# Kernel tuning notes

Hardware: AMD Instinct MI355X
Metric: run time of the kernel (lower is better)

## Reference

```python
import jax, jax.numpy as jnp
import numpy as np

L, D, B, S = 131072, 512, 512, 512


def setup_inputs() -> dict:
    key = jax.random.key(0)
    k0, k1, k2, k3 = jax.random.split(key, 4)
    stdv = 1.0 / np.sqrt(D).astype(np.float32)
    inp = jax.random.normal(k0, (B, D), jnp.float32)
    labels = jax.random.normal(k1, (L, D), jnp.float32) * 0.05  # aggregated label embeddings 'v'
    weight = jax.random.uniform(k2, (L, D), jnp.float32, -stdv, stdv)  # refinement vectors 'u'
    alpha = jnp.zeros((1, D), jnp.float32)
    beta = jnp.zeros((1, D), jnp.float32)
    bias = jnp.zeros((L,), jnp.float32)
    shortlist = jax.random.randint(k3, (B, S), 0, L, dtype=jnp.int64)
    return {"input": inp, "labels": labels, "weight": weight,
            "alpha": alpha, "beta": beta, "bias": bias, "shortlist": shortlist}


def reference(input, labels, weight, alpha, beta, bias, shortlist):
    # sigmoid-gated combine of refinement vector u and label embedding v: [L, D]
    lbl_clf = jax.nn.sigmoid(alpha) * weight + jax.nn.sigmoid(beta) * labels
    # shortlist gather: [B, S, D] and [B, S]
    clf = lbl_clf[shortlist]
    b = bias[shortlist]
    # per-sample batched dot products: [B, S]
    out = jnp.einsum('bd,bsd->bs', input, clf) + b
    return out
```

## Files before the change

kernel.cpp:

```cpp
#include <hip/hip_runtime.h>


#define D_DIM 512
#define S_DIM 512

__global__ void combine_uv_kernel(
    const float* __restrict__ input,
    const float* __restrict__ labels,
    const float* __restrict__ weight,
    const float* __restrict__ alpha,
    const float* __restrict__ beta,
    const float* __restrict__ bias,
    const int* __restrict__ shortlist,
    float* __restrict__ out)
{
    __shared__ float ga[D_DIM];
    __shared__ float gb[D_DIM];
    __shared__ int sl[64];

    const int b   = blockIdx.x;
    const int s0  = blockIdx.y * 64;
    const int tid = threadIdx.x;

    for (int d = tid; d < D_DIM; d += 256) {
        float x  = input[b * D_DIM + d];
        float sa = 1.0f / (1.0f + __expf(-alpha[d]));
        float sb = 1.0f / (1.0f + __expf(-beta[d]));
        ga[d] = x * sa;
        gb[d] = x * sb;
    }
    if (tid < 64) sl[tid] = shortlist[b * S_DIM + s0 + tid];
    __syncthreads();

    const int wave = tid >> 6;
    const int lane = tid & 63;

    float a0[4], a1[4], b0v[4], b1v[4];
    #pragma unroll
    for (int k = 0; k < 4; ++k) {
        a0[k]  = ga[lane * 4 + k];
        a1[k]  = ga[256 + lane * 4 + k];
        b0v[k] = gb[lane * 4 + k];
        b1v[k] = gb[256 + lane * 4 + k];
    }

    for (int j = 0; j < 16; j += 2) {
        const int si0 = wave * 16 + j;
        const int si1 = si0 + 1;
        const long long l0 = (long long)sl[si0];
        const long long l1 = (long long)sl[si1];

        const float4* w0 = (const float4*)(weight + l0 * D_DIM);
        const float4* v0 = (const float4*)(labels + l0 * D_DIM);
        const float4* w1 = (const float4*)(weight + l1 * D_DIM);
        const float4* v1 = (const float4*)(labels + l1 * D_DIM);

        float4 w0a = w0[lane];      float4 w0b = w0[64 + lane];
        float4 v0a = v0[lane];      float4 v0b = v0[64 + lane];
        float4 w1a = w1[lane];      float4 w1b = w1[64 + lane];
        float4 v1a = v1[lane];      float4 v1b = v1[64 + lane];

        float acc0 = w0a.x * a0[0] + w0a.y * a0[1] + w0a.z * a0[2] + w0a.w * a0[3]
                   + w0b.x * a1[0] + w0b.y * a1[1] + w0b.z * a1[2] + w0b.w * a1[3]
                   + v0a.x * b0v[0] + v0a.y * b0v[1] + v0a.z * b0v[2] + v0a.w * b0v[3]
                   + v0b.x * b1v[0] + v0b.y * b1v[1] + v0b.z * b1v[2] + v0b.w * b1v[3];

        float acc1 = w1a.x * a0[0] + w1a.y * a0[1] + w1a.z * a0[2] + w1a.w * a0[3]
                   + w1b.x * a1[0] + w1b.y * a1[1] + w1b.z * a1[2] + w1b.w * a1[3]
                   + v1a.x * b0v[0] + v1a.y * b0v[1] + v1a.z * b0v[2] + v1a.w * b0v[3]
                   + v1b.x * b1v[0] + v1b.y * b1v[1] + v1b.z * b1v[2] + v1b.w * b1v[3];

        #pragma unroll
        for (int off = 32; off > 0; off >>= 1) {
            acc0 += __shfl_down(acc0, off, 64);
            acc1 += __shfl_down(acc1, off, 64);
        }

        if (lane == 0) {
            out[b * S_DIM + s0 + si0] = acc0 + bias[l0];
            out[b * S_DIM + s0 + si1] = acc1 + bias[l1];
        }
    }
}

extern "C" void kernel_launch(void* const* d_in, const int* in_sizes, int n_in,
                              void* d_out, int out_size, void* d_ws, size_t ws_size,
                              hipStream_t stream) {
    const float* input     = (const float*)d_in[0];
    const float* labels    = (const float*)d_in[1];
    const float* weight    = (const float*)d_in[2];
    const float* alpha     = (const float*)d_in[3];
    const float* beta      = (const float*)d_in[4];
    const float* bias      = (const float*)d_in[5];
    const int* shortlist   = (const int*)d_in[6];
    float* out             = (float*)d_out;

    const int B = 512;
    const int S = 512;
    dim3 grid(B, S / 64);
    dim3 block(256);
    combine_uv_kernel<<<grid, block, 0, stream>>>(
        input, labels, weight, alpha, beta, bias, shortlist, out);
}
```

Baseline: 571.6 us.

## Split each wave into 16-lane groups handling four shortlist rows concurrently

```diff
diff --git a/kernel.cpp b/kernel.cpp
--- a/kernel.cpp
+++ b/kernel.cpp
@@ -4,7 +4,8 @@
 #define D_DIM 512
 #define S_DIM 512
 
-__global__ void combine_uv_kernel(
+__global__ __launch_bounds__(256, 4)
+void combine_uv_kernel(
     const float* __restrict__ input,
     const float* __restrict__ labels,
     const float* __restrict__ weight,
@@ -16,7 +17,8 @@
 {
     __shared__ float ga[D_DIM];
     __shared__ float gb[D_DIM];
-    __shared__ int sl[64];
+    __shared__ int   sl[64];
+    __shared__ float bb[64];
 
     const int b   = blockIdx.x;
     const int s0  = blockIdx.y * 64;
@@ -29,57 +31,52 @@
         ga[d] = x * sa;
         gb[d] = x * sb;
     }
-    if (tid < 64) sl[tid] = shortlist[b * S_DIM + s0 + tid];
+    if (tid < 64) {
+        const int l = shortlist[b * S_DIM + s0 + tid];
+        sl[tid] = l;
+        bb[tid] = bias[l];
+    }
     __syncthreads();
 
     const int wave = tid >> 6;
     const int lane = tid & 63;
+    const int g    = lane >> 4;
+    const int m    = lane & 15;
 
-    float a0[4], a1[4], b0v[4], b1v[4];
+    const float4* gaf = (const float4*)ga;
+    const float4* gbf = (const float4*)gb;
+
     #pragma unroll
-    for (int k = 0; k < 4; ++k) {
-        a0[k]  = ga[lane * 4 + k];
-        a1[k]  = ga[256 + lane * 4 + k];
-        b0v[k] = gb[lane * 4 + k];
-        b1v[k] = gb[256 + lane * 4 + k];
-    }
+    for (int i = 0; i < 4; ++i) {
+        const int    si = wave * 16 + i * 4 + g;
+        const size_t l  = (size_t)sl[si];
+        const float4* wrow = (const float4*)(weight + l * D_DIM);
+        const float4* vrow = (const float4*)(labels + l * D_DIM);
 
-    for (int j = 0; j < 16; j += 2) {
-        const int si0 = wave * 16 + j;
-        const int si1 = si0 + 1;
-        const long long l0 = (long long)sl[si0];
-        const long long l1 = (long long)sl[si1];
+        float4 wd[8], vd[8];
+        #pragma unroll
+        for (int k = 0; k < 8; ++k) wd[k] = wrow[m + 16 * k];
+        #pragma unroll
+        for (int k = 0; k < 8; ++k) vd[k] = vrow[m + 16 * k];
 
-        const float4* w0 = (const float4*)(weight + l0 * D_DIM);
-        const float4* v0 = (const float4*)(labels + l0 * D_DIM);
-        const float4* w1 = (const float4*)(weight + l1 * D_DIM);
-        const float4* v1 = (const float4*)(labels + l1 * D_DIM);
-
-        float4 w0a = w0[lane];      float4 w0b = w0[64 + lane];
-        float4 v0a = v0[lane];      float4 v0b = v0[64 + lane];
-        float4 w1a = w1[lane];      float4 w1b = w1[64 + lane];
-        float4 v1a = v1[lane];      float4 v1b = v1[64 + lane];
-
-        float acc0 = w0a.x * a0[0] + w0a.y * a0[1] + w0a.z * a0[2] + w0a.w * a0[3]
-                   + w0b.x * a1[0] + w0b.y * a1[1] + w0b.z * a1[2] + w0b.w * a1[3]
-                   + v0a.x * b0v[0] + v0a.y * b0v[1] + v0a.z * b0v[2] + v0a.w * b0v[3]
-                   + v0b.x * b1v[0] + v0b.y * b1v[1] + v0b.z * b1v[2] + v0b.w * b1v[3];
-
-        float acc1 = w1a.x * a0[0] + w1a.y * a0[1] + w1a.z * a0[2] + w1a.w * a0[3]
-                   + w1b.x * a1[0] + w1b.y * a1[1] + w1b.z * a1[2] + w1b.w * a1[3]
-                   + v1a.x * b0v[0] + v1a.y * b0v[1] + v1a.z * b0v[2] + v1a.w * b0v[3]
-                   + v1b.x * b1v[0] + v1b.y * b1v[1] + v1b.z * b1v[2] + v1b.w * b1v[3];
-
+        float acc = 0.0f;
         #pragma unroll
-        for (int off = 32; off > 0; off >>= 1) {
-            acc0 += __shfl_down(acc0, off, 64);
-            acc1 += __shfl_down(acc1, off, 64);
+        for (int k = 0; k < 8; ++k) {
+            const float4 a = gaf[m + 16 * k];
+            acc += wd[k].x * a.x + wd[k].y * a.y + wd[k].z * a.z + wd[k].w * a.w;
+        }
+        #pragma unroll
+        for (int k = 0; k < 8; ++k) {
+            const float4 c = gbf[m + 16 * k];
+            acc += vd[k].x * c.x + vd[k].y * c.y + vd[k].z * c.z + vd[k].w * c.w;
         }
 
-        if (lane == 0) {
-            out[b * S_DIM + s0 + si0] = acc0 + bias[l0];
-            out[b * S_DIM + s0 + si1] = acc1 + bias[l1];
-        }
+        acc += __shfl_xor(acc, 8, 64);
+        acc += __shfl_xor(acc, 4, 64);
+        acc += __shfl_xor(acc, 2, 64);
+        acc += __shfl_xor(acc, 1, 64);
+
+        if (m == 0) out[b * S_DIM + s0 + si] = acc + bb[si];
     }
 }
 
```

Result: no change. 567.1 us (-0.8%).
